# Kernel tuning notes

Hardware: AMD Instinct MI355X
Metric: run time of the kernel (lower is better)

The kernel has to match this reference:

```python
import jax, jax.numpy as jnp
import numpy as np

BLANK_ID = 0


def bias_norm(x, bias, log_scale):
    # icefall BiasNorm: x * exp(log_scale) / rms(x - bias), rms over channel dim
    scales = jnp.exp(log_scale) * jax.lax.rsqrt(
        jnp.mean(jnp.square(x - bias), axis=-1, keepdims=True))
    return x * scales


def setup_inputs() -> dict:
    key = jax.random.key(0)
    N, T, S = 16, 400, 5
    ENC, DEC, JOINT, V = 512, 512, 512, 2000
    OV = V - 1  # out_vocab_dim
    ks = jax.random.split(key, 16)
    f = jax.random.normal
    return {
        "encoder_out": f(ks[0], (N, T, S, ENC), jnp.float32),
        "blank_decoder_out": f(ks[1], (N, T, S, DEC), jnp.float32),
        "vocab_decoder_out": f(ks[2], (N, T, S, DEC), jnp.float32),
        # fc_encoder_proj + its BiasNorm
        "W_enc": f(ks[3], (JOINT, ENC), jnp.float32) * 0.02,
        "b_enc": jnp.zeros((JOINT,), jnp.float32),
        "bn_enc_bias": f(ks[4], (JOINT,), jnp.float32) * 0.01,
        "bn_enc_log_scale": jnp.zeros((), jnp.float32),
        # fc_blank_decoder + its BiasNorm
        "W_bdec": f(ks[5], (JOINT, DEC), jnp.float32) * 0.02,
        "b_bdec": jnp.zeros((JOINT,), jnp.float32),
        "bn_bdec_bias": f(ks[6], (JOINT,), jnp.float32) * 0.01,
        "bn_bdec_log_scale": jnp.zeros((), jnp.float32),
        # BiasNorm for vocab decoder path (over decoder_hidden_dim)
        "bn_vdec_bias": f(ks[7], (DEC,), jnp.float32) * 0.01,
        "bn_vdec_log_scale": jnp.zeros((), jnp.float32),
        # output heads
        "W_blank": f(ks[8], (1, JOINT), jnp.float32) * 0.02,
        "b_blank": jnp.zeros((1,), jnp.float32),
        "W_ev": f(ks[9], (OV, JOINT), jnp.float32) * 0.02,
        "b_ev": jnp.zeros((OV,), jnp.float32),
        "W_dv": f(ks[10], (OV, JOINT), jnp.float32) * 0.02,
        "b_dv": jnp.zeros((OV,), jnp.float32),
    }


def reference(encoder_out, blank_decoder_out, vocab_decoder_out,
              W_enc, b_enc, bn_enc_bias, bn_enc_log_scale,
              W_bdec, b_bdec, bn_bdec_bias, bn_bdec_log_scale,
              bn_vdec_bias, bn_vdec_log_scale,
              W_blank, b_blank, W_ev, b_ev, W_dv, b_dv):
    # encoder_proj: ScaledLinear -> BiasNorm
    enc = bias_norm(jnp.einsum('ntsc,jc->ntsj', encoder_out, W_enc) + b_enc,
                    bn_enc_bias, bn_enc_log_scale)
    # blank_decoder_proj: ScaledLinear -> BiasNorm
    bdec = bias_norm(jnp.einsum('ntsc,jc->ntsj', blank_decoder_out, W_bdec) + b_bdec,
                     bn_bdec_bias, bn_bdec_log_scale)
    # vocab_decoder_proj: BiasNorm -> ScaledLinear -> log_softmax
    vdec = bias_norm(vocab_decoder_out, bn_vdec_bias, bn_vdec_log_scale)
    vdec = jnp.einsum('ntsj,vj->ntsv', vdec, W_dv) + b_dv
    vocab_decoder_prob = jax.nn.log_softmax(vdec, axis=-1)
    # joint
    blank_prob = jnp.einsum('ntsj,oj->ntso', jax.nn.relu(enc + bdec), W_blank) + b_blank
    vocab_prob = jnp.einsum('ntsj,vj->ntsv', enc, W_ev) + b_ev + vocab_decoder_prob
    out = jnp.concatenate(
        [vocab_prob[..., :BLANK_ID], blank_prob, vocab_prob[..., BLANK_ID:]], axis=-1)
    return out, vocab_decoder_prob
```

## Files before the change

### kernel.cpp

```cpp
#include <hip/hip_runtime.h>


#define R_TOTAL 32000
#define OV 1999

typedef __attribute__((ext_vector_type(8))) short bh8;
typedef __attribute__((ext_vector_type(4))) float fx4;

__device__ __forceinline__ unsigned short f2bf(float f) {
  union { float f; unsigned u; } v; v.f = f;
  unsigned r = v.u + 0x7fffu + ((v.u >> 16) & 1u);
  return (unsigned short)(r >> 16);
}
__device__ __forceinline__ float bf2f(unsigned short h) {
  union { unsigned u; float f; } v; v.u = ((unsigned)h) << 16;
  return v.f;
}
__device__ __forceinline__ void gload_lds16(const void* g, void* l) {
  __builtin_amdgcn_global_load_lds(
      (__attribute__((address_space(1))) void*)g,
      (__attribute__((address_space(3))) void*)l, 16, 0, 0);
}

__global__ void wconv_kernel(const float* __restrict__ src, unsigned short* __restrict__ dst,
                             int src_rows, int dst_rows) {
  long long n = (long long)dst_rows * 512;
  for (long long i = (long long)blockIdx.x * blockDim.x + threadIdx.x; i < n;
       i += (long long)gridDim.x * blockDim.x) {
    int row = (int)(i >> 9);
    dst[i] = (row < src_rows) ? f2bf(src[i]) : (unsigned short)0;
  }
}

template<int MODE>
__global__ __launch_bounds__(512, 2)
void proj_norm_kernel(const float* __restrict__ X,
                      const unsigned short* __restrict__ Wb,
                      const float* __restrict__ b_lin,
                      const float* __restrict__ bn_bias,
                      const float* __restrict__ log_scale,
                      unsigned short* __restrict__ enc_b,
                      const float* __restrict__ W_blank,
                      const float* __restrict__ b_blank,
                      float* __restrict__ outp)
{
  __shared__ unsigned short As[128 * 64];
  __shared__ unsigned short Bs[512 * 64];
  __shared__ float red[4][128];
  __shared__ float scale_s[128];

  const int tid = threadIdx.x;
  const int l  = tid & 63;
  const int lq = l >> 4;
  const int lr = l & 15;
  const int w  = tid >> 6;
  const int wr = w >> 2;
  const int wc = w & 3;
  const int rowBase = blockIdx.x * 128;

  char* AsB = (char*)As;
  char* BsB = (char*)Bs;

  fx4 acc[4][8];
#pragma unroll
  for (int m = 0; m < 4; ++m)
#pragma unroll
    for (int n = 0; n < 8; ++n)
#pragma unroll
      for (int r = 0; r < 4; ++r) acc[m][n][r] = 0.f;

  for (int kt = 0; kt < 8; ++kt) {
#pragma unroll
    for (int p = 0; p < 4; ++p) {
      int g = tid + p * 512;
      int row = g >> 4;
      int c4  = g & 15;
      const float4 v = *(const float4*)(X + (long long)(rowBase + row) * 512 + kt * 64 + c4 * 4);
      ushort4 h;
      h.x = f2bf(v.x); h.y = f2bf(v.y); h.z = f2bf(v.z); h.w = f2bf(v.w);
      *(ushort4*)(AsB + row * 128 + ((c4 * 8) ^ ((row & 7) << 4))) = h;
    }
#pragma unroll
    for (int p = 0; p < 8; ++p) {
      int gb = (w * 8 + p) * 64;
      int g = gb + l;
      int row = g >> 3;
      int c8 = (g & 7) ^ (row & 7);
      gload_lds16(Wb + (long long)row * 512 + kt * 64 + c8 * 8, BsB + gb * 16);
    }
    __syncthreads();

#pragma unroll
    for (int kk = 0; kk < 2; ++kk) {
      const int kb = (kk * 32 + lq * 8) * 2;
      bh8 a[4];
#pragma unroll
      for (int m = 0; m < 4; ++m) {
        int row = wr * 64 + m * 16 + lr;
        a[m] = *(const bh8*)(AsB + row * 128 + (kb ^ ((row & 7) << 4)));
      }
#pragma unroll
      for (int n = 0; n < 8; ++n) {
        int brow = wc * 128 + n * 16 + lr;
        bh8 bfr = *(const bh8*)(BsB + brow * 128 + (kb ^ ((brow & 7) << 4)));
#pragma unroll
        for (int m = 0; m < 4; ++m)
          acc[m][n] = __builtin_amdgcn_mfma_f32_16x16x32_bf16(a[m], bfr, acc[m][n], 0, 0, 0);
      }
    }
    __syncthreads();
  }

  const float escale = expf(log_scale[0]);
  float bl[8], bb[8], wb[8];
#pragma unroll
  for (int n = 0; n < 8; ++n) {
    int col = wc * 128 + n * 16 + lr;
    bl[n] = b_lin[col];
    bb[n] = bn_bias[col];
    if (MODE == 1) wb[n] = W_blank[col];
  }

  float ps[4][4];
#pragma unroll
  for (int m = 0; m < 4; ++m)
#pragma unroll
    for (int r = 0; r < 4; ++r) ps[m][r] = 0.f;
#pragma unroll
  for (int m = 0; m < 4; ++m)
#pragma unroll
    for (int n = 0; n < 8; ++n)
#pragma unroll
      for (int r = 0; r < 4; ++r) {
        float v = acc[m][n][r] + bl[n];
        float d = v - bb[n];
        ps[m][r] += d * d;
      }
#pragma unroll
  for (int off = 1; off < 16; off <<= 1)
#pragma unroll
    for (int m = 0; m < 4; ++m)
#pragma unroll
      for (int r = 0; r < 4; ++r)
        ps[m][r] += __shfl_xor(ps[m][r], off);

  if (lr == 0) {
#pragma unroll
    for (int m = 0; m < 4; ++m)
#pragma unroll
      for (int r = 0; r < 4; ++r)
        red[wc][wr * 64 + m * 16 + lq * 4 + r] = ps[m][r];
  }
  __syncthreads();
  if (tid < 128) {
    float s = red[0][tid] + red[1][tid] + red[2][tid] + red[3][tid];
    scale_s[tid] = escale * rsqrtf(s * (1.0f / 512.0f));
  }
  __syncthreads();

  if (MODE == 0) {
#pragma unroll
    for (int m = 0; m < 4; ++m)
#pragma unroll
      for (int n = 0; n < 8; ++n)
#pragma unroll
        for (int r = 0; r < 4; ++r) {
          int rl = wr * 64 + m * 16 + lq * 4 + r;
          int col = wc * 128 + n * 16 + lr;
          float v = (acc[m][n][r] + bl[n]) * scale_s[rl];
          enc_b[(long long)(rowBase + rl) * 512 + col] = f2bf(v);
        }
  } else {
    float pb[4][4];
#pragma unroll
    for (int m = 0; m < 4; ++m)
#pragma unroll
      for (int r = 0; r < 4; ++r) pb[m][r] = 0.f;
#pragma unroll
    for (int m = 0; m < 4; ++m)
#pragma unroll
      for (int n = 0; n < 8; ++n)
#pragma unroll
        for (int r = 0; r < 4; ++r) {
          int rl = wr * 64 + m * 16 + lq * 4 + r;
          int col = wc * 128 + n * 16 + lr;
          float v = (acc[m][n][r] + bl[n]) * scale_s[rl];
          float e = bf2f(enc_b[(long long)(rowBase + rl) * 512 + col]);
          float s = e + v;
          s = s > 0.f ? s : 0.f;
          pb[m][r] += s * wb[n];
        }
#pragma unroll
    for (int off = 1; off < 16; off <<= 1)
#pragma unroll
      for (int m = 0; m < 4; ++m)
#pragma unroll
        for (int r = 0; r < 4; ++r)
          pb[m][r] += __shfl_xor(pb[m][r], off);
    if (lr == 0) {
#pragma unroll
      for (int m = 0; m < 4; ++m)
#pragma unroll
        for (int r = 0; r < 4; ++r)
          red[wc][wr * 64 + m * 16 + lq * 4 + r] = pb[m][r];
    }
    __syncthreads();
    if (tid < 128)
      outp[(long long)(rowBase + tid) * 2000] =
          red[0][tid] + red[1][tid] + red[2][tid] + red[3][tid] + b_blank[0];
  }
}

__global__ __launch_bounds__(256)
void vdec_norm_kernel(const float* __restrict__ X, const float* __restrict__ bn_bias,
                      const float* __restrict__ log_scale, unsigned short* __restrict__ dst)
{
  const int l = threadIdx.x & 63;
  const long long row = (long long)blockIdx.x * 4 + (threadIdx.x >> 6);
  const float* xr = X + row * 512 + l * 8;
  float4 v0 = *(const float4*)xr;
  float4 v1 = *(const float4*)(xr + 4);
  float xv[8] = {v0.x, v0.y, v0.z, v0.w, v1.x, v1.y, v1.z, v1.w};
  const float4 b0 = *(const float4*)(bn_bias + l * 8);
  const float4 b1 = *(const float4*)(bn_bias + l * 8 + 4);
  float bv[8] = {b0.x, b0.y, b0.z, b0.w, b1.x, b1.y, b1.z, b1.w};
  float s = 0.f;
#pragma unroll
  for (int i = 0; i < 8; ++i) { float d = xv[i] - bv[i]; s += d * d; }
#pragma unroll
  for (int off = 1; off < 64; off <<= 1) s += __shfl_xor(s, off);
  const float sc = expf(log_scale[0]) * rsqrtf(s * (1.0f / 512.0f));
  bh8 o;
#pragma unroll
  for (int i = 0; i < 8; ++i) o[i] = (short)f2bf(xv[i] * sc);
  *(bh8*)(dst + row * 512 + l * 8) = o;
}

template<int MODE>
__global__ __launch_bounds__(256, 2)
void gemm_out_kernel(const unsigned short* __restrict__ Abf,
                     const unsigned short* __restrict__ Wb,
                     const float* __restrict__ bias,
                     const float* __restrict__ vdp,
                     float* __restrict__ dstf)
{
  __shared__ unsigned short As[128 * 64];
  __shared__ unsigned short Bs[128 * 64];
  const int tid = threadIdx.x;
  const int l  = tid & 63, lq = l >> 4, lr = l & 15;
  const int w  = tid >> 6;
  const int wr = w >> 1, wc = w & 1;
  const int rowBase = blockIdx.x * 128;
  const int colBase = blockIdx.y * 128;
  char* AsB = (char*)As;
  char* BsB = (char*)Bs;

  fx4 acc[4][4];
#pragma unroll
  for (int m = 0; m < 4; ++m)
#pragma unroll
    for (int n = 0; n < 4; ++n)
#pragma unroll
      for (int r = 0; r < 4; ++r) acc[m][n][r] = 0.f;

  for (int kt = 0; kt < 8; ++kt) {
#pragma unroll
    for (int p = 0; p < 4; ++p) {
      int gb = (w * 4 + p) * 64;
      int g = gb + l;
      int row = g >> 3;
      int c8 = (g & 7) ^ (row & 7);
      gload_lds16(Abf + (long long)(rowBase + row) * 512 + kt * 64 + c8 * 8, AsB + gb * 16);
      gload_lds16(Wb  + (long long)(colBase + row) * 512 + kt * 64 + c8 * 8, BsB + gb * 16);
    }
    __syncthreads();
#pragma unroll
    for (int kk = 0; kk < 2; ++kk) {
      const int kb = (kk * 32 + lq * 8) * 2;
      bh8 a[4];
#pragma unroll
      for (int m = 0; m < 4; ++m) {
        int row = wr * 64 + m * 16 + lr;
        a[m] = *(const bh8*)(AsB + row * 128 + (kb ^ ((row & 7) << 4)));
      }
#pragma unroll
      for (int n = 0; n < 4; ++n) {
        int brow = wc * 64 + n * 16 + lr;
        bh8 bfr = *(const bh8*)(BsB + brow * 128 + (kb ^ ((brow & 7) << 4)));
#pragma unroll
        for (int m = 0; m < 4; ++m)
          acc[m][n] = __builtin_amdgcn_mfma_f32_16x16x32_bf16(a[m], bfr, acc[m][n], 0, 0, 0);
      }
    }
    __syncthreads();
  }

#pragma unroll
  for (int n = 0; n < 4; ++n) {
    int col = colBase + wc * 64 + n * 16 + lr;
    if (col < OV) {
      float bc = bias[col];
#pragma unroll
      for (int m = 0; m < 4; ++m)
#pragma unroll
        for (int r = 0; r < 4; ++r) {
          long long rg = rowBase + wr * 64 + m * 16 + lq * 4 + r;
          float v = acc[m][n][r] + bc;
          if (MODE == 0) dstf[rg * OV + col] = v;
          else           dstf[rg * 2000 + 1 + col] = v + vdp[rg * OV + col];
        }
    }
  }
}

__global__ __launch_bounds__(256)
void lsm_kernel(float* __restrict__ vdp)
{
  const long long r = blockIdx.x;
  float* row = vdp + r * OV;
  const int t = threadIdx.x;
  const int w = t >> 6;
  __shared__ float sm[4], ss[4];
  float v[8];
  float mx = -3.4e38f;
#pragma unroll
  for (int i = 0; i < 8; ++i) {
    int idx = i * 256 + t;
    v[i] = (idx < OV) ? row[idx] : -3.4e38f;
    mx = fmaxf(mx, v[i]);
  }
#pragma unroll
  for (int off = 1; off < 64; off <<= 1) mx = fmaxf(mx, __shfl_xor(mx, off));
  if ((t & 63) == 0) sm[w] = mx;
  __syncthreads();
  mx = fmaxf(fmaxf(sm[0], sm[1]), fmaxf(sm[2], sm[3]));
  float s = 0.f;
#pragma unroll
  for (int i = 0; i < 8; ++i) s += expf(v[i] - mx);
  ;
#pragma unroll
  for (int off = 1; off < 64; off <<= 1) s += __shfl_xor(s, off);
  if ((t & 63) == 0) ss[w] = s;
  __syncthreads();
  s = ss[0] + ss[1] + ss[2] + ss[3];
  const float lz = mx + logf(s);
#pragma unroll
  for (int i = 0; i < 8; ++i) {
    int idx = i * 256 + t;
    if (idx < OV) row[idx] = v[i] - lz;
  }
}

extern "C" void kernel_launch(void* const* d_in, const int* in_sizes, int n_in,
                              void* d_out, int out_size, void* d_ws, size_t ws_size,
                              hipStream_t stream) {
  const float* encoder_out  = (const float*)d_in[0];
  const float* blank_dec    = (const float*)d_in[1];
  const float* vocab_dec    = (const float*)d_in[2];
  const float* W_enc        = (const float*)d_in[3];
  const float* b_enc        = (const float*)d_in[4];
  const float* bn_enc_bias  = (const float*)d_in[5];
  const float* bn_enc_ls    = (const float*)d_in[6];
  const float* W_bdec       = (const float*)d_in[7];
  const float* b_bdec       = (const float*)d_in[8];
  const float* bn_bdec_bias = (const float*)d_in[9];
  const float* bn_bdec_ls   = (const float*)d_in[10];
  const float* bn_vdec_bias = (const float*)d_in[11];
  const float* bn_vdec_ls   = (const float*)d_in[12];
  const float* W_blank      = (const float*)d_in[13];
  const float* b_blank      = (const float*)d_in[14];
  const float* W_ev         = (const float*)d_in[15];
  const float* b_ev         = (const float*)d_in[16];
  const float* W_dv         = (const float*)d_in[17];
  const float* b_dv         = (const float*)d_in[18];

  unsigned short* Wenc_b  = (unsigned short*)d_ws;
  unsigned short* Wbdec_b = Wenc_b + 512 * 512;
  unsigned short* Wdv_b   = Wbdec_b + 512 * 512;
  unsigned short* Wev_b   = Wdv_b + 2048 * 512;
  unsigned short* enc_b   = Wev_b + 2048 * 512;
  unsigned short* vdec_b  = enc_b + (size_t)R_TOTAL * 512;

  float* outp = (float*)d_out;
  float* vdp  = outp + (size_t)R_TOTAL * 2000;

  wconv_kernel<<<256, 256, 0, stream>>>(W_enc,  Wenc_b,  512, 512);
  wconv_kernel<<<256, 256, 0, stream>>>(W_bdec, Wbdec_b, 512, 512);
  wconv_kernel<<<512, 256, 0, stream>>>(W_dv,   Wdv_b,  1999, 2048);
  wconv_kernel<<<512, 256, 0, stream>>>(W_ev,   Wev_b,  1999, 2048);

  proj_norm_kernel<0><<<250, 512, 0, stream>>>(encoder_out, Wenc_b, b_enc, bn_enc_bias,
                                               bn_enc_ls, enc_b, nullptr, nullptr, nullptr);
  proj_norm_kernel<1><<<250, 512, 0, stream>>>(blank_dec, Wbdec_b, b_bdec, bn_bdec_bias,
                                               bn_bdec_ls, enc_b, W_blank, b_blank, outp);
  vdec_norm_kernel<<<8000, 256, 0, stream>>>(vocab_dec, bn_vdec_bias, bn_vdec_ls, vdec_b);

  gemm_out_kernel<0><<<dim3(250, 16), 256, 0, stream>>>(vdec_b, Wdv_b, b_dv, nullptr, vdp);
  lsm_kernel<<<32000, 256, 0, stream>>>(vdp);
  gemm_out_kernel<1><<<dim3(250, 16), 256, 0, stream>>>(enc_b, Wev_b, b_ev, vdp, outp);
}
```

Measured before the change: 632.5 us.

## Fuse log-softmax stats into vocab GEMM epilogue and widen projection blocks

The vocab-decoder GEMM now computes per-tile row max and sum-exp in its epilogue and writes them to a stats buffer. A small kernel merges the 16 partial stats per row into a log-normalizer. The final GEMM subtracts it while adding the decoder term, which removes the separate full-row log-softmax pass over vdp. The projection kernels also move to 1024-thread blocks with 8 column waves, which reduces per-thread accumulators but drops the 2-blocks-per-CU launch bound.

```diff
diff --git a/kernel.cpp b/kernel.cpp
--- a/kernel.cpp
+++ b/kernel.cpp
@@ -33,7 +33,7 @@
 }
 
 template<int MODE>
-__global__ __launch_bounds__(512, 2)
+__global__ __launch_bounds__(1024)
 void proj_norm_kernel(const float* __restrict__ X,
                       const unsigned short* __restrict__ Wb,
                       const float* __restrict__ b_lin,
@@ -46,7 +46,7 @@
 {
   __shared__ unsigned short As[128 * 64];
   __shared__ unsigned short Bs[512 * 64];
-  __shared__ float red[4][128];
+  __shared__ float red[8][128];
   __shared__ float scale_s[128];
 
   const int tid = threadIdx.x;
@@ -54,25 +54,25 @@
   const int lq = l >> 4;
   const int lr = l & 15;
   const int w  = tid >> 6;
-  const int wr = w >> 2;
-  const int wc = w & 3;
+  const int wr = w >> 3;
+  const int wc = w & 7;
   const int rowBase = blockIdx.x * 128;
 
   char* AsB = (char*)As;
   char* BsB = (char*)Bs;
 
-  fx4 acc[4][8];
-#pragma unroll
-  for (int m = 0; m < 4; ++m)
-#pragma unroll
-    for (int n = 0; n < 8; ++n)
+  fx4 acc[4][4];
+#pragma unroll
+  for (int m = 0; m < 4; ++m)
+#pragma unroll
+    for (int n = 0; n < 4; ++n)
 #pragma unroll
       for (int r = 0; r < 4; ++r) acc[m][n][r] = 0.f;
 
   for (int kt = 0; kt < 8; ++kt) {
 #pragma unroll
-    for (int p = 0; p < 4; ++p) {
-      int g = tid + p * 512;
+    for (int p = 0; p < 2; ++p) {
+      int g = tid + p * 1024;
       int row = g >> 4;
       int c4  = g & 15;
       const float4 v = *(const float4*)(X + (long long)(rowBase + row) * 512 + kt * 64 + c4 * 4);
@@ -81,8 +81,8 @@
       *(ushort4*)(AsB + row * 128 + ((c4 * 8) ^ ((row & 7) << 4))) = h;
     }
 #pragma unroll
-    for (int p = 0; p < 8; ++p) {
-      int gb = (w * 8 + p) * 64;
+    for (int p = 0; p < 4; ++p) {
+      int gb = (w * 4 + p) * 64;
       int g = gb + l;
       int row = g >> 3;
       int c8 = (g & 7) ^ (row & 7);
@@ -100,8 +100,8 @@
         a[m] = *(const bh8*)(AsB + row * 128 + (kb ^ ((row & 7) << 4)));
       }
 #pragma unroll
-      for (int n = 0; n < 8; ++n) {
-        int brow = wc * 128 + n * 16 + lr;
+      for (int n = 0; n < 4; ++n) {
+        int brow = wc * 64 + n * 16 + lr;
         bh8 bfr = *(const bh8*)(BsB + brow * 128 + (kb ^ ((brow & 7) << 4)));
 #pragma unroll
         for (int m = 0; m < 4; ++m)
@@ -112,10 +112,10 @@
   }
 
   const float escale = expf(log_scale[0]);
-  float bl[8], bb[8], wb[8];
-#pragma unroll
-  for (int n = 0; n < 8; ++n) {
-    int col = wc * 128 + n * 16 + lr;
+  float bl[4], bb[4], wb[4];
+#pragma unroll
+  for (int n = 0; n < 4; ++n) {
+    int col = wc * 64 + n * 16 + lr;
     bl[n] = b_lin[col];
     bb[n] = bn_bias[col];
     if (MODE == 1) wb[n] = W_blank[col];
@@ -129,7 +129,7 @@
 #pragma unroll
   for (int m = 0; m < 4; ++m)
 #pragma unroll
-    for (int n = 0; n < 8; ++n)
+    for (int n = 0; n < 4; ++n)
 #pragma unroll
       for (int r = 0; r < 4; ++r) {
         float v = acc[m][n][r] + bl[n];
@@ -153,7 +153,9 @@
   }
   __syncthreads();
   if (tid < 128) {
-    float s = red[0][tid] + red[1][tid] + red[2][tid] + red[3][tid];
+    float s = 0.f;
+#pragma unroll
+    for (int c = 0; c < 8; ++c) s += red[c][tid];
     scale_s[tid] = escale * rsqrtf(s * (1.0f / 512.0f));
   }
   __syncthreads();
@@ -162,11 +164,11 @@
 #pragma unroll
     for (int m = 0; m < 4; ++m)
 #pragma unroll
-      for (int n = 0; n < 8; ++n)
+      for (int n = 0; n < 4; ++n)
 #pragma unroll
         for (int r = 0; r < 4; ++r) {
           int rl = wr * 64 + m * 16 + lq * 4 + r;
-          int col = wc * 128 + n * 16 + lr;
+          int col = wc * 64 + n * 16 + lr;
           float v = (acc[m][n][r] + bl[n]) * scale_s[rl];
           enc_b[(long long)(rowBase + rl) * 512 + col] = f2bf(v);
         }
@@ -179,11 +181,11 @@
 #pragma unroll
     for (int m = 0; m < 4; ++m)
 #pragma unroll
-      for (int n = 0; n < 8; ++n)
+      for (int n = 0; n < 4; ++n)
 #pragma unroll
         for (int r = 0; r < 4; ++r) {
           int rl = wr * 64 + m * 16 + lq * 4 + r;
-          int col = wc * 128 + n * 16 + lr;
+          int col = wc * 64 + n * 16 + lr;
           float v = (acc[m][n][r] + bl[n]) * scale_s[rl];
           float e = bf2f(enc_b[(long long)(rowBase + rl) * 512 + col]);
           float s = e + v;
@@ -205,9 +207,12 @@
           red[wc][wr * 64 + m * 16 + lq * 4 + r] = pb[m][r];
     }
     __syncthreads();
-    if (tid < 128)
-      outp[(long long)(rowBase + tid) * 2000] =
-          red[0][tid] + red[1][tid] + red[2][tid] + red[3][tid] + b_blank[0];
+    if (tid < 128) {
+      float s = 0.f;
+#pragma unroll
+      for (int c = 0; c < 8; ++c) s += red[c][tid];
+      outp[(long long)(rowBase + tid) * 2000] = s + b_blank[0];
+    }
   }
 }
 
@@ -236,13 +241,177 @@
   *(bh8*)(dst + row * 512 + l * 8) = o;
 }
 
-template<int MODE>
 __global__ __launch_bounds__(256, 2)
-void gemm_out_kernel(const unsigned short* __restrict__ Abf,
+void gemm_vl_kernel(const unsigned short* __restrict__ Abf,
+                    const unsigned short* __restrict__ Wb,
+                    const float* __restrict__ bias,
+                    float* __restrict__ vdp,
+                    float2* __restrict__ stats)
+{
+  __shared__ unsigned short As[128 * 64];
+  __shared__ unsigned short Bs[128 * 64];
+  __shared__ float smax[2][128];
+  __shared__ float ssum[2][128];
+  const int tid = threadIdx.x;
+  const int l  = tid & 63, lq = l >> 4, lr = l & 15;
+  const int w  = tid >> 6;
+  const int wr = w >> 1, wc = w & 1;
+  const int rowBase = blockIdx.x * 128;
+  const int colBase = blockIdx.y * 128;
+  char* AsB = (char*)As;
+  char* BsB = (char*)Bs;
+
+  fx4 acc[4][4];
+#pragma unroll
+  for (int m = 0; m < 4; ++m)
+#pragma unroll
+    for (int n = 0; n < 4; ++n)
+#pragma unroll
+      for (int r = 0; r < 4; ++r) acc[m][n][r] = 0.f;
+
+  for (int kt = 0; kt < 8; ++kt) {
+#pragma unroll
+    for (int p = 0; p < 4; ++p) {
+      int gb = (w * 4 + p) * 64;
+      int g = gb + l;
+      int row = g >> 3;
+      int c8 = (g & 7) ^ (row & 7);
+      gload_lds16(Abf + (long long)(rowBase + row) * 512 + kt * 64 + c8 * 8, AsB + gb * 16);
+      gload_lds16(Wb  + (long long)(colBase + row) * 512 + kt * 64 + c8 * 8, BsB + gb * 16);
+    }
+    __syncthreads();
+#pragma unroll
+    for (int kk = 0; kk < 2; ++kk) {
+      const int kb = (kk * 32 + lq * 8) * 2;
+      bh8 a[4];
+#pragma unroll
+      for (int m = 0; m < 4; ++m) {
+        int row = wr * 64 + m * 16 + lr;
+        a[m] = *(const bh8*)(AsB + row * 128 + (kb ^ ((row & 7) << 4)));
+      }
+#pragma unroll
+      for (int n = 0; n < 4; ++n) {
+        int brow = wc * 64 + n * 16 + lr;
+        bh8 bfr = *(const bh8*)(BsB + brow * 128 + (kb ^ ((brow & 7) << 4)));
+#pragma unroll
+        for (int m = 0; m < 4; ++m)
+          acc[m][n] = __builtin_amdgcn_mfma_f32_16x16x32_bf16(a[m], bfr, acc[m][n], 0, 0, 0);
+      }
+    }
+    __syncthreads();
+  }
+
+  float bl[4]; bool cv[4];
+#pragma unroll
+  for (int n = 0; n < 4; ++n) {
+    int col = colBase + wc * 64 + n * 16 + lr;
+    cv[n] = (col < OV);
+    bl[n] = cv[n] ? bias[col] : 0.f;
+  }
+
+  float mloc[4][4];
+#pragma unroll
+  for (int m = 0; m < 4; ++m)
+#pragma unroll
+    for (int r = 0; r < 4; ++r) mloc[m][r] = -3.4e38f;
+#pragma unroll
+  for (int m = 0; m < 4; ++m)
+#pragma unroll
+    for (int n = 0; n < 4; ++n)
+      if (cv[n])
+#pragma unroll
+        for (int r = 0; r < 4; ++r)
+          mloc[m][r] = fmaxf(mloc[m][r], acc[m][n][r] + bl[n]);
+#pragma unroll
+  for (int off = 1; off < 16; off <<= 1)
+#pragma unroll
+    for (int m = 0; m < 4; ++m)
+#pragma unroll
+      for (int r = 0; r < 4; ++r)
+        mloc[m][r] = fmaxf(mloc[m][r], __shfl_xor(mloc[m][r], off));
+  if (lr == 0) {
+#pragma unroll
+    for (int m = 0; m < 4; ++m)
+#pragma unroll
+      for (int r = 0; r < 4; ++r)
+        smax[wc][wr * 64 + m * 16 + lq * 4 + r] = mloc[m][r];
+  }
+  __syncthreads();
+  float M[4][4];
+#pragma unroll
+  for (int m = 0; m < 4; ++m)
+#pragma unroll
+    for (int r = 0; r < 4; ++r) {
+      int row = wr * 64 + m * 16 + lq * 4 + r;
+      M[m][r] = fmaxf(smax[0][row], smax[1][row]);
+    }
+  float sl[4][4];
+#pragma unroll
+  for (int m = 0; m < 4; ++m)
+#pragma unroll
+    for (int r = 0; r < 4; ++r) sl[m][r] = 0.f;
+#pragma unroll
+  for (int m = 0; m < 4; ++m)
+#pragma unroll
+    for (int n = 0; n < 4; ++n)
+      if (cv[n]) {
+        int col = colBase + wc * 64 + n * 16 + lr;
+#pragma unroll
+        for (int r = 0; r < 4; ++r) {
+          float v = acc[m][n][r] + bl[n];
+          sl[m][r] += __expf(v - M[m][r]);
+          long long rg = rowBase + wr * 64 + m * 16 + lq * 4 + r;
+          vdp[rg * OV + col] = v;
+        }
+      }
+#pragma unroll
+  for (int off = 1; off < 16; off <<= 1)
+#pragma unroll
+    for (int m = 0; m < 4; ++m)
+#pragma unroll
+      for (int r = 0; r < 4; ++r)
+        sl[m][r] += __shfl_xor(sl[m][r], off);
+  if (lr == 0) {
+#pragma unroll
+    for (int m = 0; m < 4; ++m)
+#pragma unroll
+      for (int r = 0; r < 4; ++r)
+        ssum[wc][wr * 64 + m * 16 + lq * 4 + r] = sl[m][r];
+  }
+  __syncthreads();
+  if (tid < 128) {
+    float2 st;
+    st.x = fmaxf(smax[0][tid], smax[1][tid]);
+    st.y = ssum[0][tid] + ssum[1][tid];
+    stats[(long long)(rowBase + tid) * 16 + blockIdx.y] = st;
+  }
+}
+
+__global__ __launch_bounds__(256)
+void lz_kernel(const float2* __restrict__ stats, float* __restrict__ lz)
+{
+  int row = blockIdx.x * 256 + threadIdx.x;
+  if (row >= R_TOTAL) return;
+  float2 st[16];
+  float M = -3.4e38f;
+#pragma unroll
+  for (int i = 0; i < 16; ++i) {
+    st[i] = stats[(long long)row * 16 + i];
+    M = fmaxf(M, st[i].x);
+  }
+  float S = 0.f;
+#pragma unroll
+  for (int i = 0; i < 16; ++i) S += st[i].y * __expf(st[i].x - M);
+  lz[row] = M + logf(S);
+}
+
+__global__ __launch_bounds__(256, 2)
+void gemm_fin_kernel(const unsigned short* __restrict__ Abf,
                      const unsigned short* __restrict__ Wb,
                      const float* __restrict__ bias,
-                     const float* __restrict__ vdp,
-                     float* __restrict__ dstf)
+                     const float* __restrict__ lz,
+                     float* __restrict__ vdp,
+                     float* __restrict__ outp)
 {
   __shared__ unsigned short As[128 * 64];
   __shared__ unsigned short Bs[128 * 64];
@@ -295,6 +464,13 @@
     __syncthreads();
   }
 
+  float lzv[4][4];
+#pragma unroll
+  for (int m = 0; m < 4; ++m)
+#pragma unroll
+    for (int r = 0; r < 4; ++r)
+      lzv[m][r] = lz[rowBase + wr * 64 + m * 16 + lq * 4 + r];
+
 #pragma unroll
   for (int n = 0; n < 4; ++n) {
     int col = colBase + wc * 64 + n * 16 + lr;
@@ -305,49 +481,12 @@
 #pragma unroll
         for (int r = 0; r < 4; ++r) {
           long long rg = rowBase + wr * 64 + m * 16 + lq * 4 + r;
-          float v = acc[m][n][r] + bc;
-          if (MODE == 0) dstf[rg * OV + col] = v;
-          else           dstf[rg * 2000 + 1 + col] = v + vdp[rg * OV + col];
+          float raw = vdp[rg * OV + col];
+          float vd = raw - lzv[m][r];
+          vdp[rg * OV + col] = vd;
+          outp[rg * 2000 + 1 + col] = acc[m][n][r] + bc + vd;
         }
     }
-  }
-}
-
-__global__ __launch_bounds__(256)
-void lsm_kernel(float* __restrict__ vdp)
-{
-  const long long r = blockIdx.x;
-  float* row = vdp + r * OV;
-  const int t = threadIdx.x;
-  const int w = t >> 6;
-  __shared__ float sm[4], ss[4];
-  float v[8];
-  float mx = -3.4e38f;
-#pragma unroll
-  for (int i = 0; i < 8; ++i) {
-    int idx = i * 256 + t;
-    v[i] = (idx < OV) ? row[idx] : -3.4e38f;
-    mx = fmaxf(mx, v[i]);
-  }
-#pragma unroll
-  for (int off = 1; off < 64; off <<= 1) mx = fmaxf(mx, __shfl_xor(mx, off));
-  if ((t & 63) == 0) sm[w] = mx;
-  __syncthreads();
-  mx = fmaxf(fmaxf(sm[0], sm[1]), fmaxf(sm[2], sm[3]));
-  float s = 0.f;
-#pragma unroll
-  for (int i = 0; i < 8; ++i) s += expf(v[i] - mx);
-  ;
-#pragma unroll
-  for (int off = 1; off < 64; off <<= 1) s += __shfl_xor(s, off);
-  if ((t & 63) == 0) ss[w] = s;
-  __syncthreads();
-  s = ss[0] + ss[1] + ss[2] + ss[3];
-  const float lz = mx + logf(s);
-#pragma unroll
-  for (int i = 0; i < 8; ++i) {
-    int idx = i * 256 + t;
-    if (idx < OV) row[idx] = v[i] - lz;
   }
 }
 
@@ -380,6 +519,8 @@
   unsigned short* Wev_b   = Wdv_b + 2048 * 512;
   unsigned short* enc_b   = Wev_b + 2048 * 512;
   unsigned short* vdec_b  = enc_b + (size_t)R_TOTAL * 512;
+  float2* stats = (float2*)(vdec_b + (size_t)R_TOTAL * 512);
+  float*  lzbuf = (float*)(stats + (size_t)R_TOTAL * 16);
 
   float* outp = (float*)d_out;
   float* vdp  = outp + (size_t)R_TOTAL * 2000;
@@ -389,13 +530,13 @@
   wconv_kernel<<<512, 256, 0, stream>>>(W_dv,   Wdv_b,  1999, 2048);
   wconv_kernel<<<512, 256, 0, stream>>>(W_ev,   Wev_b,  1999, 2048);
 
-  proj_norm_kernel<0><<<250, 512, 0, stream>>>(encoder_out, Wenc_b, b_enc, bn_enc_bias,
-                                               bn_enc_ls, enc_b, nullptr, nullptr, nullptr);
-  proj_norm_kernel<1><<<250, 512, 0, stream>>>(blank_dec, Wbdec_b, b_bdec, bn_bdec_bias,
-                                               bn_bdec_ls, enc_b, W_blank, b_blank, outp);
+  proj_norm_kernel<0><<<250, 1024, 0, stream>>>(encoder_out, Wenc_b, b_enc, bn_enc_bias,
+                                                bn_enc_ls, enc_b, nullptr, nullptr, nullptr);
+  proj_norm_kernel<1><<<250, 1024, 0, stream>>>(blank_dec, Wbdec_b, b_bdec, bn_bdec_bias,
+                                                bn_bdec_ls, enc_b, W_blank, b_blank, outp);
   vdec_norm_kernel<<<8000, 256, 0, stream>>>(vocab_dec, bn_vdec_bias, bn_vdec_ls, vdec_b);
 
-  gemm_out_kernel<0><<<dim3(250, 16), 256, 0, stream>>>(vdec_b, Wdv_b, b_dv, nullptr, vdp);
-  lsm_kernel<<<32000, 256, 0, stream>>>(vdp);
-  gemm_out_kernel<1><<<dim3(250, 16), 256, 0, stream>>>(enc_b, Wev_b, b_ev, vdp, outp);
-}
+  gemm_vl_kernel<<<dim3(250, 16), 256, 0, stream>>>(vdec_b, Wdv_b, b_dv, vdp, stats);
+  lz_kernel<<<125, 256, 0, stream>>>(stats, lzbuf);
+  gemm_fin_kernel<<<dim3(250, 16), 256, 0, stream>>>(enc_b, Wev_b, b_ev, lzbuf, vdp, outp);
+}
```

Result: slower. 710.6 us (+12.3%).
